# Performance work log

Hardware: AMD Instinct MI355X
Metric: run time of the kernel (lower is better)

## Reference

```python
import jax, jax.numpy as jnp
import numpy as np
import math

B, N, D, H, K, HID, FF = 4, 4096, 256, 4, 16, 64, 1024
DH = D // H
EPS = 1e-5


def setup_inputs() -> dict:
    key = jax.random.key(0)
    ks = jax.random.split(key, 24)
    s = 0.02
    inp = {
        'xyz': jax.random.uniform(ks[0], (B, N, 3), dtype=jnp.float32),
        'feats': jax.random.normal(ks[1], (B, N, D), dtype=jnp.float32),
        'ln_q_g': jnp.ones((D,), jnp.float32),
        'ln_q_b': jnp.zeros((D,), jnp.float32),
        'Wq': jax.random.normal(ks[2], (D, D), jnp.float32) * s,
        'bq': jnp.zeros((D,), jnp.float32),
        'Wk': jax.random.normal(ks[3], (D, D), jnp.float32) * s,
        'bk': jnp.zeros((D,), jnp.float32),
        'Wv': jax.random.normal(ks[4], (D, D), jnp.float32) * s,
        'bv': jnp.zeros((D,), jnp.float32),
        'W_rel1': jax.random.normal(ks[5], (4, HID), jnp.float32) * s,
        'b_rel1': jnp.zeros((HID,), jnp.float32),
        'W_rel2': jax.random.normal(ks[6], (HID, D), jnp.float32) * s,
        'b_rel2': jnp.zeros((D,), jnp.float32),
        'Wo': jax.random.normal(ks[7], (D, D), jnp.float32) * s,
        'bo': jnp.zeros((D,), jnp.float32),
        'ln_f_g': jnp.ones((D,), jnp.float32),
        'ln_f_b': jnp.zeros((D,), jnp.float32),
        'W_ff1': jax.random.normal(ks[8], (D, FF), jnp.float32) * s,
        'b_ff1': jnp.zeros((FF,), jnp.float32),
        'W_ff2': jax.random.normal(ks[9], (FF, D), jnp.float32) * s,
        'b_ff2': jnp.zeros((D,), jnp.float32),
    }
    return inp


def _layernorm(x, g, b):
    mu = jnp.mean(x, axis=-1, keepdims=True)
    var = jnp.var(x, axis=-1, keepdims=True)
    return (x - mu) * jax.lax.rsqrt(var + EPS) * g + b


def _knn_indices(xyz, k):
    # pairwise squared distances (B, N, N); exclude self via +inf diagonal
    sq = jnp.sum(xyz * xyz, axis=-1)  # (B, N)
    d2 = sq[:, :, None] + sq[:, None, :] - 2.0 * jnp.einsum('bnc,bmc->bnm', xyz, xyz)
    d2 = d2 + jnp.eye(xyz.shape[1], dtype=xyz.dtype) * 1e9
    _, idx = jax.lax.top_k(-d2, k)  # (B, N, k) nearest neighbors
    return idx


def _index_points(pts, idx):
    # pts: (B, N, C), idx: (B, N, k) -> (B, N, k, C)
    return jax.vmap(lambda p, i: p[i])(pts, idx)


def reference(xyz, feats, ln_q_g, ln_q_b, Wq, bq, Wk, bk, Wv, bv,
              W_rel1, b_rel1, W_rel2, b_rel2, Wo, bo,
              ln_f_g, ln_f_b, W_ff1, b_ff1, W_ff2, b_ff2):
    k = min(K, N - 1)
    idx = _knn_indices(xyz, k)

    x = _layernorm(feats, ln_q_g, ln_q_b)
    q = x @ Wq + bq
    k_lin = x @ Wk + bk
    v_lin = x @ Wv + bv

    k_nb = _index_points(k_lin, idx)   # (B,N,k,D)
    v_nb = _index_points(v_lin, idx)   # (B,N,k,D)
    nb_xyz = _index_points(xyz, idx)   # (B,N,k,3)

    diff = nb_xyz - xyz[:, :, None, :]
    rel = jnp.concatenate([diff, jnp.linalg.norm(diff, axis=-1, keepdims=True)], axis=-1)  # (B,N,k,4)
    rel_e = jax.nn.gelu(rel @ W_rel1 + b_rel1, approximate=False) @ W_rel2 + b_rel2

    k_nb = k_nb + rel_e
    v_nb = v_nb + rel_e

    qh = q.reshape(B, N, H, DH)              # (B,N,H,dh)
    kh = k_nb.reshape(B, N, k, H, DH)        # (B,N,k,H,dh)
    vh = v_nb.reshape(B, N, k, H, DH)

    attn = jnp.einsum('bnhc,bnkhc->bnhk', qh, kh) / math.sqrt(DH)
    attn = jax.nn.softmax(attn, axis=-1)
    out = jnp.einsum('bnhk,bnkhc->bnhc', attn, vh).reshape(B, N, D)
    out = out @ Wo + bo

    feats = feats + out
    h = _layernorm(feats, ln_f_g, ln_f_b)
    h = jax.nn.gelu(h @ W_ff1 + b_ff1, approximate=False) @ W_ff2 + b_ff2
    return feats + h
```

## Files before the change

kernel.cpp:

```cpp
#include <hip/hip_runtime.h>
#include <hip/hip_bf16.h>
#include <math.h>

#define NB 4
#define NPTS 4096
#define DIM 256
#define KNN 16
#define HID 64
#define FFDIM 1024
#define LN_EPS 1e-5f
#define MTOT (NB * NPTS)
#define KINF 3e38f
#define QPB 8

typedef __attribute__((ext_vector_type(8))) short short8;
typedef __attribute__((ext_vector_type(4))) float f32x4;

__device__ __forceinline__ float gelu_f(float x) {
    return 0.5f * x * (1.0f + erff(x * 0.7071067811865476f));
}
__device__ __forceinline__ float b2f(ushort u) {
    return __uint_as_float(((unsigned)u) << 16);
}
__device__ __forceinline__ ushort f2b(float f) {
    unsigned u = __float_as_uint(f);
    return (ushort)((u + 0x7fffu + ((u >> 16) & 1u)) >> 16);
}
__device__ __forceinline__ void gload16(const void* g, void* l) {
    __builtin_amdgcn_global_load_lds((const __attribute__((address_space(1))) void*)g,
                                     (__attribute__((address_space(3))) void*)l, 16, 0, 0);
}
__device__ __forceinline__ float dot8(uint4 w, const float* q) {
    float s = 0.f;
    s += b2f((ushort)(w.x & 0xffff)) * q[0]; s += b2f((ushort)(w.x >> 16)) * q[1];
    s += b2f((ushort)(w.y & 0xffff)) * q[2]; s += b2f((ushort)(w.y >> 16)) * q[3];
    s += b2f((ushort)(w.z & 0xffff)) * q[4]; s += b2f((ushort)(w.z >> 16)) * q[5];
    s += b2f((ushort)(w.w & 0xffff)) * q[6]; s += b2f((ushort)(w.w >> 16)) * q[7];
    return s;
}

__global__ __launch_bounds__(256) void knn_kernel(const float* __restrict__ xyz,
                                                  int* __restrict__ idx_out) {
    int blk = blockIdx.x;
    int bq0 = blk * QPB;
    int b = bq0 >> 12;
    const float* base = xyz + (size_t)b * NPTS * 3;
    int t = threadIdx.x;
    int lane = t & 63, wv = t >> 6;

    __shared__ float wq0S[64];
    __shared__ float wq1S[64];
    __shared__ int   cnt[QPB];
    __shared__ float cV[QPB][64];
    __shared__ int   cI[QPB][64];

    if (t < QPB) cnt[t] = 0;

    float px[16], py[16], pz[16], sq[16];
    #pragma unroll
    for (int i = 0; i < 16; ++i) {
        int m = t + 256 * i;
        px[i] = base[m * 3 + 0];
        py[i] = base[m * 3 + 1];
        pz[i] = base[m * 3 + 2];
        sq[i] = px[i] * px[i] + py[i] * py[i] + pz[i] * pz[i];
    }
    __syncthreads();

    #pragma unroll 1
    for (int qp = 0; qp < QPB; qp += 2) {
        int n0 = (bq0 + qp)     & (NPTS - 1);
        int n1 = (bq0 + qp + 1) & (NPTS - 1);
        float q0x = base[n0 * 3 + 0], q0y = base[n0 * 3 + 1], q0z = base[n0 * 3 + 2];
        float q1x = base[n1 * 3 + 0], q1y = base[n1 * 3 + 1], q1z = base[n1 * 3 + 2];
        float sq0 = q0x * q0x + q0y * q0y + q0z * q0z;
        float sq1 = q1x * q1x + q1y * q1y + q1z * q1z;

        float d0[16], d1[16];
        #pragma unroll
        for (int i = 0; i < 16; ++i) {
            int m = t + 256 * i;
            float dot0 = px[i] * q0x + py[i] * q0y + pz[i] * q0z;
            float dot1 = px[i] * q1x + py[i] * q1y + pz[i] * q1z;
            float dd0 = (sq0 + sq[i]) - 2.0f * dot0;
            float dd1 = (sq1 + sq[i]) - 2.0f * dot1;
            d0[i] = (m == n0) ? KINF : dd0;
            d1[i] = (m == n1) ? KINF : dd1;
        }
        float lm0 = d0[0], lm1 = d1[0];
        #pragma unroll
        for (int i = 1; i < 16; ++i) { lm0 = fminf(lm0, d0[i]); lm1 = fminf(lm1, d1[i]); }

        float v0 = lm0, v1 = lm1;
        #pragma unroll
        for (int k = 2; k <= 64; k <<= 1) {
            #pragma unroll
            for (int j = 32; j > 0; j >>= 1) {
                if (j < k) {
                    float ov0 = __shfl_xor(v0, j, 64);
                    float ov1 = __shfl_xor(v1, j, 64);
                    bool keepMin = ((lane & k) == 0) == ((lane & j) == 0);
                    if (keepMin == (ov0 < v0)) v0 = ov0;
                    if (keepMin == (ov1 < v1)) v1 = ov1;
                }
            }
        }
        if (lane < 16) { wq0S[wv * 16 + lane] = v0; wq1S[wv * 16 + lane] = v1; }
        __syncthreads();

        float s0 = wq0S[lane], s1 = wq1S[lane];
        #pragma unroll
        for (int k = 2; k <= 64; k <<= 1) {
            #pragma unroll
            for (int j = 32; j > 0; j >>= 1) {
                if (j < k) {
                    float os0 = __shfl_xor(s0, j, 64);
                    float os1 = __shfl_xor(s1, j, 64);
                    bool keepMin = ((lane & k) == 0) == ((lane & j) == 0);
                    if (keepMin == (os0 < s0)) s0 = os0;
                    if (keepMin == (os1 < s1)) s1 = os1;
                }
            }
        }
        float T0 = __shfl(s0, 15, 64);
        float T1 = __shfl(s1, 15, 64);

        #pragma unroll
        for (int i = 0; i < 16; ++i) {
            if (d0[i] <= T0) {
                int pos = atomicAdd(&cnt[qp], 1);
                if (pos < 64) { cV[qp][pos] = d0[i]; cI[qp][pos] = t + 256 * i; }
            }
        }
        #pragma unroll
        for (int i = 0; i < 16; ++i) {
            if (d1[i] <= T1) {
                int pos = atomicAdd(&cnt[qp + 1], 1);
                if (pos < 64) { cV[qp + 1][pos] = d1[i]; cI[qp + 1][pos] = t + 256 * i; }
            }
        }
        __syncthreads();
    }

    #pragma unroll
    for (int rep = 0; rep < 2; ++rep) {
        int qi = wv + 4 * rep;
        int nc = cnt[qi]; nc = nc > 64 ? 64 : nc;
        float v = (lane < nc) ? cV[qi][lane] : KINF;
        int   m = (lane < nc) ? cI[qi][lane] : 0x7fffffff;
        #pragma unroll
        for (int k = 2; k <= 64; k <<= 1) {
            #pragma unroll
            for (int j = 32; j > 0; j >>= 1) {
                if (j < k) {
                    float ov = __shfl_xor(v, j, 64);
                    int   om = __shfl_xor(m, j, 64);
                    bool keepMin = ((lane & k) == 0) == ((lane & j) == 0);
                    bool less = (ov < v) || (ov == v && om < m);
                    if (keepMin == less) { v = ov; m = om; }
                }
            }
        }
        if (lane < KNN) idx_out[(size_t)(bq0 + qi) * KNN + lane] = m;
    }
}

__global__ __launch_bounds__(256) void ln_kernel(const float* __restrict__ in,
                                                 const float* __restrict__ g,
                                                 const float* __restrict__ bb,
                                                 ushort* __restrict__ out) {
    int r = blockIdx.x;
    int t = threadIdx.x;
    float v = in[(size_t)r * DIM + t];

    __shared__ float sw[4];
    __shared__ float sw2[4];

    float s = v;
    #pragma unroll
    for (int off = 32; off > 0; off >>= 1) s += __shfl_down(s, off);
    if ((t & 63) == 0) sw[t >> 6] = s;
    __syncthreads();
    float mean = (sw[0] + sw[1] + sw[2] + sw[3]) * (1.0f / DIM);

    float dlt = v - mean;
    float s2 = dlt * dlt;
    #pragma unroll
    for (int off = 32; off > 0; off >>= 1) s2 += __shfl_down(s2, off);
    if ((t & 63) == 0) sw2[t >> 6] = s2;
    __syncthreads();
    float var = (sw2[0] + sw2[1] + sw2[2] + sw2[3]) * (1.0f / DIM);

    out[(size_t)r * DIM + t] = f2b(dlt * rsqrtf(var + LN_EPS) * g[t] + bb[t]);
}

__global__ __launch_bounds__(256) void tconv4(const float* __restrict__ s0,
                                              const float* __restrict__ s1,
                                              const float* __restrict__ s2,
                                              const float* __restrict__ s3,
                                              ushort* __restrict__ d0,
                                              ushort* __restrict__ d1,
                                              ushort* __restrict__ d2,
                                              ushort* __restrict__ d3) {
    const float* in; ushort* out;
    switch (blockIdx.z) {
        case 0: in = s0; out = d0; break;
        case 1: in = s1; out = d1; break;
        case 2: in = s2; out = d2; break;
        default: in = s3; out = d3; break;
    }
    __shared__ float tile[32][33];
    int tx = threadIdx.x & 31, ty = threadIdx.x >> 5;
    int r0 = blockIdx.y * 32, c0 = blockIdx.x * 32;
    #pragma unroll
    for (int k = 0; k < 4; ++k)
        tile[ty + 8 * k][tx] = in[(size_t)(r0 + ty + 8 * k) * 256 + c0 + tx];
    __syncthreads();
    #pragma unroll
    for (int k = 0; k < 4; ++k)
        out[(size_t)(c0 + ty + 8 * k) * 256 + r0 + tx] = f2b(tile[tx][ty + 8 * k]);
}

__global__ __launch_bounds__(256) void tconv(const float* __restrict__ in,
                                             ushort* __restrict__ out, int R, int C) {
    __shared__ float tile[32][33];
    int tx = threadIdx.x & 31, ty = threadIdx.x >> 5;
    int r0 = blockIdx.y * 32, c0 = blockIdx.x * 32;
    #pragma unroll
    for (int k = 0; k < 4; ++k)
        tile[ty + 8 * k][tx] = in[(size_t)(r0 + ty + 8 * k) * C + c0 + tx];
    __syncthreads();
    #pragma unroll
    for (int k = 0; k < 4; ++k)
        out[(size_t)(c0 + ty + 8 * k) * R + r0 + tx] = f2b(tile[tx][ty + 8 * k]);
}

__global__ __launch_bounds__(256) void prep_mats(const float* __restrict__ W2,
                                                 const float* __restrict__ Wq,
                                                 const ushort* __restrict__ WoT,
                                                 ushort* __restrict__ w2bd,
                                                 ushort* __restrict__ Wq_bf,
                                                 ushort* __restrict__ BtCat) {
    int bb = blockIdx.x, t = threadIdx.x;
    if (bb < 256) {
        float v = ((t >> 6) == (bb >> 6)) ? W2[(bb & 63) * 256 + t] : 0.0f;
        w2bd[bb * 256 + t] = f2b(v);
    } else if (bb < 512) {
        int r = bb - 256;
        Wq_bf[r * 256 + t] = f2b(Wq[r * 256 + t]);
    } else {
        int r = bb - 512;
        BtCat[(size_t)r * 512 + t] = WoT[r * 256 + t];
    }
}

__global__ __launch_bounds__(256) void prep_bias(const float* __restrict__ bq,
                                                 const float* __restrict__ bk,
                                                 const float* __restrict__ bv,
                                                 const float* __restrict__ W2,
                                                 const float* __restrict__ bo,
                                                 const float* __restrict__ br2,
                                                 const float* __restrict__ Wo,
                                                 float* __restrict__ bqkvw,
                                                 float* __restrict__ boc) {
    int bb = blockIdx.x, t = threadIdx.x;
    if (bb == 0) bqkvw[t] = bq[t];
    else if (bb == 1) bqkvw[256 + t] = bk[t];
    else if (bb == 2) bqkvw[512 + t] = bv[t];
    else if (bb == 3) {
        int h = t >> 6, i = t & 63;
        float s = 0.f;
        #pragma unroll 8
        for (int dp = 0; dp < 64; ++dp) s += bq[h * 64 + dp] * W2[i * 256 + h * 64 + dp];
        bqkvw[768 + t] = s;
    } else {
        float s = bo[t];
        #pragma unroll 8
        for (int d = 0; d < 256; ++d) s += br2[d] * Wo[d * 256 + t];
        boc[t] = s;
    }
}

template <int ACT, int OUTBF, int RES>
__global__ __launch_bounds__(256) void gemm_bt(
    const ushort* __restrict__ A, const ushort* __restrict__ Bt,
    const float* __restrict__ bias, const float* __restrict__ res,
    void* __restrict__ Cv, int M, int N, int K, int ldc)
{
    __shared__ ushort As[4096];
    __shared__ ushort Bs[4096];
    const int t = threadIdx.x;
    const int wave = t >> 6, lane = t & 63;
    const int m0 = blockIdx.y * 128, n0 = blockIdx.x * 128;
    const int wr = (wave >> 1) * 64, wc = (wave & 1) * 64;

    f32x4 acc[4][4];
    #pragma unroll
    for (int i = 0; i < 4; ++i)
        #pragma unroll
        for (int j = 0; j < 4; ++j) acc[i][j] = {0.f, 0.f, 0.f, 0.f};

    const int rA0 = (wave * 2 + 0) * 16 + (lane >> 2);
    const int rA1 = (wave * 2 + 1) * 16 + (lane >> 2);
    const int u4 = lane & 3;
    const int sw0 = (rA0 + (rA0 >> 2)) & 3;
    const int sw1 = (rA1 + (rA1 >> 2)) & 3;
    char* ldsA0 = (char*)As + (wave * 2 + 0) * 1024 + lane * 16;
    char* ldsA1 = (char*)As + (wave * 2 + 1) * 1024 + lane * 16;
    char* ldsB0 = (char*)Bs + (wave * 2 + 0) * 1024 + lane * 16;
    char* ldsB1 = (char*)Bs + (wave * 2 + 1) * 1024 + lane * 16;
    const size_t aOff0 = (size_t)(m0 + rA0) * K + (size_t)((u4 ^ sw0) * 8);
    const size_t aOff1 = (size_t)(m0 + rA1) * K + (size_t)((u4 ^ sw1) * 8);
    const size_t bOff0 = (size_t)(n0 + rA0) * K + (size_t)((u4 ^ sw0) * 8);
    const size_t bOff1 = (size_t)(n0 + rA1) * K + (size_t)((u4 ^ sw1) * 8);

    const int cl = lane & 15, gq = lane >> 4;

    for (int k0 = 0; k0 < K; k0 += 32) {
        gload16(A + aOff0 + k0, ldsA0);
        gload16(A + aOff1 + k0, ldsA1);
        gload16(Bt + bOff0 + k0, ldsB0);
        gload16(Bt + bOff1 + k0, ldsB1);
        __syncthreads();

        short8 av[4], bv[4];
        #pragma unroll
        for (int mi = 0; mi < 4; ++mi) {
            int row = wr + mi * 16 + cl;
            int s = (row + (row >> 2)) & 3;
            av[mi] = *(const short8*)((const char*)As + row * 64 + ((gq ^ s) << 4));
            int rowb = wc + mi * 16 + cl;
            int sb = (rowb + (rowb >> 2)) & 3;
            bv[mi] = *(const short8*)((const char*)Bs + rowb * 64 + ((gq ^ sb) << 4));
        }
        #pragma unroll
        for (int mi = 0; mi < 4; ++mi)
            #pragma unroll
            for (int ni = 0; ni < 4; ++ni)
                acc[mi][ni] = __builtin_amdgcn_mfma_f32_16x16x32_bf16(av[mi], bv[ni], acc[mi][ni], 0, 0, 0);
        __syncthreads();
    }

    float* Cf = (float*)Cv;
    ushort* Cb = (ushort*)Cv;
    #pragma unroll
    for (int ni = 0; ni < 4; ++ni) {
        int col = n0 + wc + ni * 16 + cl;
        float bvv = bias ? bias[col] : 0.0f;
        #pragma unroll
        for (int mi = 0; mi < 4; ++mi) {
            #pragma unroll
            for (int r = 0; r < 4; ++r) {
                int row = m0 + wr + mi * 16 + gq * 4 + r;
                float v = acc[mi][ni][r] + bvv;
                if (ACT == 1) v = gelu_f(v);
                if (RES) v += res[(size_t)row * N + col];
                if (OUTBF) Cb[(size_t)row * ldc + col] = f2b(v);
                else       Cf[(size_t)row * ldc + col] = v;
            }
        }
    }
}

#define PTS 8
__global__ __launch_bounds__(256) void attn_kernel(
    const int* __restrict__ idx,
    const ushort* __restrict__ qkvw,
    const float* __restrict__ xyz,
    const float* __restrict__ W1,
    const float* __restrict__ b1,
    ushort* __restrict__ ab)
{
    __shared__ float qS[256];
    __shared__ float qwS[256];
    __shared__ float psS[64];
    __shared__ uint4 hidS4[16 * 9];
    __shared__ int   nbAll[128];
    __shared__ float w1S[256];
    __shared__ float b1S[64];
    ushort* hidS = (ushort*)hidS4;

    const int t = threadIdx.x;
    const int h = t >> 6, lane = t & 63;
    const int bid = blockIdx.x;
    const int blk = ((bid & 7) << 8) | (bid >> 3);
    const int bn0 = blk * PTS;
    const int R0 = blk * (PTS * 16);

    if (t < 128) nbAll[t] = idx[R0 + t];
    w1S[t] = W1[t];
    if (t < 64) b1S[t] = b1[t];
    const float* xb3 = xyz + (size_t)(bn0 >> 12) * NPTS * 3;
    __syncthreads();

    for (int pt = 0; pt < PTS; ++pt) {
        const int bn = bn0 + pt;
        const size_t base = (size_t)(bn >> 12) * NPTS;

        qS[t]  = b2f(qkvw[(size_t)bn * 1024 + t]);
        qwS[t] = b2f(qkvw[(size_t)bn * 1024 + 768 + t]);
        {
            int n = bn & (NPTS - 1);
            float nx = xb3[n * 3 + 0], ny = xb3[n * 3 + 1], nz = xb3[n * 3 + 2];
            int j = t >> 4;
            int i0 = (t & 15) * 4;
            int m = nbAll[pt * 16 + j];
            float dx = xb3[m * 3 + 0] - nx;
            float dy = xb3[m * 3 + 1] - ny;
            float dz = xb3[m * 3 + 2] - nz;
            float nr = sqrtf(dx * dx + dy * dy + dz * dz);
            uint2 hw;
            float a0 = b1S[i0 + 0] + dx * w1S[i0 + 0] + dy * w1S[64 + i0 + 0] + dz * w1S[128 + i0 + 0] + nr * w1S[192 + i0 + 0];
            float a1 = b1S[i0 + 1] + dx * w1S[i0 + 1] + dy * w1S[64 + i0 + 1] + dz * w1S[128 + i0 + 1] + nr * w1S[192 + i0 + 1];
            float a2 = b1S[i0 + 2] + dx * w1S[i0 + 2] + dy * w1S[64 + i0 + 2] + dz * w1S[128 + i0 + 2] + nr * w1S[192 + i0 + 2];
            float a3 = b1S[i0 + 3] + dx * w1S[i0 + 3] + dy * w1S[64 + i0 + 3] + dz * w1S[128 + i0 + 3] + nr * w1S[192 + i0 + 3];
            hw.x = (uint)f2b(gelu_f(a0)) | ((uint)f2b(gelu_f(a1)) << 16);
            hw.y = (uint)f2b(gelu_f(a2)) | ((uint)f2b(gelu_f(a3)) << 16);
            *(uint2*)(hidS + j * 72 + i0) = hw;
        }
        __syncthreads();

        {
            int j = lane >> 2, sub = lane & 3;
            int m = nbAll[pt * 16 + j];
            const ushort* krow = qkvw + (base + m) * 1024 + 256 + h * 64 + sub * 16;
            uint4 ka = *(const uint4*)krow;
            uint4 kc = *(const uint4*)(krow + 8);
            const float* qp = &qS[h * 64 + sub * 16];
            float d1 = dot8(ka, qp) + dot8(kc, qp + 8);
            const ushort* hrow = hidS + j * 72 + sub * 16;
            uint4 ha = *(const uint4*)hrow;
            uint4 hc = *(const uint4*)(hrow + 8);
            const float* qwp = &qwS[h * 64 + sub * 16];
            float d2 = dot8(ha, qwp) + dot8(hc, qwp + 8);
            float pp = d1 + d2;
            pp += __shfl_xor(pp, 1, 64);
            pp += __shfl_xor(pp, 2, 64);
            pp *= 0.125f;
            float mx = pp;
            mx = fmaxf(mx, __shfl_xor(mx, 4, 64));
            mx = fmaxf(mx, __shfl_xor(mx, 8, 64));
            mx = fmaxf(mx, __shfl_xor(mx, 16, 64));
            mx = fmaxf(mx, __shfl_xor(mx, 32, 64));
            float e = expf(pp - mx);
            float ss = e;
            ss += __shfl_xor(ss, 4, 64);
            ss += __shfl_xor(ss, 8, 64);
            ss += __shfl_xor(ss, 16, 64);
            ss += __shfl_xor(ss, 32, 64);
            float pj = e / ss;
            if (sub == 0) psS[h * 16 + j] = pj;
        }
        __syncthreads();

        {
            float o = 0.f, hpv = 0.f;
            #pragma unroll
            for (int j = 0; j < 16; ++j) {
                float p = psS[h * 16 + j];
                int m = nbAll[pt * 16 + j];
                o   += p * b2f(qkvw[(base + m) * 1024 + 512 + t]);
                hpv += p * b2f(hidS[j * 72 + lane]);
            }
            ab[(size_t)bn * 512 + t]       = f2b(o);
            ab[(size_t)bn * 512 + 256 + t] = f2b(hpv);
        }
        __syncthreads();
    }
}

extern "C" void kernel_launch(void* const* d_in, const int* in_sizes, int n_in,
                              void* d_out, int out_size, void* d_ws, size_t ws_size,
                              hipStream_t stream) {
    const float* xyz    = (const float*)d_in[0];
    const float* feats  = (const float*)d_in[1];
    const float* ln_q_g = (const float*)d_in[2];
    const float* ln_q_b = (const float*)d_in[3];
    const float* Wq     = (const float*)d_in[4];
    const float* bq     = (const float*)d_in[5];
    const float* Wk     = (const float*)d_in[6];
    const float* bk     = (const float*)d_in[7];
    const float* Wv     = (const float*)d_in[8];
    const float* bv     = (const float*)d_in[9];
    const float* W_rel1 = (const float*)d_in[10];
    const float* b_rel1 = (const float*)d_in[11];
    const float* W_rel2 = (const float*)d_in[12];
    const float* b_rel2 = (const float*)d_in[13];
    const float* Wo     = (const float*)d_in[14];
    const float* bo     = (const float*)d_in[15];
    const float* ln_f_g = (const float*)d_in[16];
    const float* ln_f_b = (const float*)d_in[17];
    const float* W_ff1  = (const float*)d_in[18];
    const float* b_ff1  = (const float*)d_in[19];
    const float* W_ff2  = (const float*)d_in[20];
    const float* b_ff2  = (const float*)d_in[21];
    (void)in_sizes; (void)n_in; (void)out_size; (void)ws_size;

    char* ws = (char*)d_ws;
    const size_t MB = 1u << 20;
    int*    idx    = (int*)ws;
    ushort* xb     = (ushort*)(ws + 1 * MB);
    ushort* qkvw   = (ushort*)(ws + 9 * MB);
    ushort* ff1b   = (ushort*)(ws + 41 * MB);
    ushort* ab     = (ushort*)(ws + 73 * MB);
    ushort* BtQKVW = (ushort*)(ws + 89 * MB);
    ushort* WoT    = BtQKVW + 262144;
    ushort* Wf1T   = WoT + 65536;
    ushort* Wf2T   = Wf1T + 262144;
    ushort* Wq_bf  = Wf2T + 262144;
    ushort* w2bd   = Wq_bf + 65536;
    ushort* BtCat  = w2bd + 65536;
    float*  bqkvw  = (float*)(BtCat + 131072);
    float*  boc    = bqkvw + 1024;
    float*  feats1 = (float*)(ws + 9 * MB);
    ushort* hb     = xb;

    tconv4<<<dim3(8, 8, 4), 256, 0, stream>>>(Wq, Wk, Wv, Wo,
                                              BtQKVW, BtQKVW + 65536, BtQKVW + 131072, WoT);
    tconv<<<dim3(32, 8), 256, 0, stream>>>(W_ff1, Wf1T, 256, 1024);
    tconv<<<dim3(8, 32), 256, 0, stream>>>(W_ff2, Wf2T, 1024, 256);
    prep_mats<<<768, 256, 0, stream>>>(W_rel2, Wq, WoT, w2bd, Wq_bf, BtCat);
    gemm_bt<0, 1, 0><<<dim3(2, 2), 256, 0, stream>>>(w2bd, Wq_bf, nullptr, nullptr,
                                                     BtQKVW + 768 * 256, 256, 256, 256, 256);
    gemm_bt<0, 1, 0><<<dim3(2, 2), 256, 0, stream>>>(WoT, w2bd, nullptr, nullptr,
                                                     BtCat + 256, 256, 256, 256, 512);
    prep_bias<<<5, 256, 0, stream>>>(bq, bk, bv, W_rel2, bo, b_rel2, Wo, bqkvw, boc);

    knn_kernel<<<MTOT / QPB, 256, 0, stream>>>(xyz, idx);
    ln_kernel<<<MTOT, 256, 0, stream>>>(feats, ln_q_g, ln_q_b, xb);

    gemm_bt<0, 1, 0><<<dim3(8, 128), 256, 0, stream>>>(xb, BtQKVW, bqkvw, nullptr,
                                                       qkvw, MTOT, 1024, 256, 1024);

    attn_kernel<<<MTOT / PTS, 256, 0, stream>>>(idx, qkvw, xyz, W_rel1, b_rel1, ab);

    gemm_bt<0, 0, 1><<<dim3(2, 128), 256, 0, stream>>>(ab, BtCat, boc, feats, feats1, MTOT, 256, 512, 256);
    ln_kernel<<<MTOT, 256, 0, stream>>>(feats1, ln_f_g, ln_f_b, hb);
    gemm_bt<1, 1, 0><<<dim3(8, 128), 256, 0, stream>>>(hb, Wf1T, b_ff1, nullptr, ff1b, MTOT, 1024, 256, 1024);
    gemm_bt<0, 0, 1><<<dim3(2, 128), 256, 0, stream>>>(ff1b, Wf2T, b_ff2, feats1, (float*)d_out, MTOT, 256, 1024, 256);
}
```

Baseline: 288.4 us.

## Restructure KNN so each wavefront computes one query's top-k from LDS-staged points

The KNN kernel now stages all of a batch's point coordinates in shared memory. Each wavefront handles a whole query on its own: it computes 64 distances per lane, finds a threshold with an in-wave bitonic sort, compacts the candidates and does the final sort. This removes the block-wide barriers and the cross-wave merge that the old paired-query loop needed. The cost is 48KB of LDS per block, which can limit occupancy. Squared norms are recomputed from LDS on every query, and each lane holds a 64-entry distance array in registers.

```diff
diff --git a/kernel.cpp b/kernel.cpp
--- a/kernel.cpp
+++ b/kernel.cpp
@@ -48,120 +48,81 @@
     int t = threadIdx.x;
     int lane = t & 63, wv = t >> 6;
 
-    __shared__ float wq0S[64];
-    __shared__ float wq1S[64];
+    __shared__ float pxS[NPTS];
+    __shared__ float pyS[NPTS];
+    __shared__ float pzS[NPTS];
     __shared__ int   cnt[QPB];
     __shared__ float cV[QPB][64];
     __shared__ int   cI[QPB][64];
 
     if (t < QPB) cnt[t] = 0;
-
-    float px[16], py[16], pz[16], sq[16];
-    #pragma unroll
-    for (int i = 0; i < 16; ++i) {
-        int m = t + 256 * i;
-        px[i] = base[m * 3 + 0];
-        py[i] = base[m * 3 + 1];
-        pz[i] = base[m * 3 + 2];
-        sq[i] = px[i] * px[i] + py[i] * py[i] + pz[i] * pz[i];
+    for (int i = t; i < NPTS; i += 256) {
+        pxS[i] = base[i * 3 + 0];
+        pyS[i] = base[i * 3 + 1];
+        pzS[i] = base[i * 3 + 2];
     }
     __syncthreads();
 
     #pragma unroll 1
-    for (int qp = 0; qp < QPB; qp += 2) {
-        int n0 = (bq0 + qp)     & (NPTS - 1);
-        int n1 = (bq0 + qp + 1) & (NPTS - 1);
-        float q0x = base[n0 * 3 + 0], q0y = base[n0 * 3 + 1], q0z = base[n0 * 3 + 2];
-        float q1x = base[n1 * 3 + 0], q1y = base[n1 * 3 + 1], q1z = base[n1 * 3 + 2];
-        float sq0 = q0x * q0x + q0y * q0y + q0z * q0z;
-        float sq1 = q1x * q1x + q1y * q1y + q1z * q1z;
-
-        float d0[16], d1[16];
-        #pragma unroll
-        for (int i = 0; i < 16; ++i) {
-            int m = t + 256 * i;
-            float dot0 = px[i] * q0x + py[i] * q0y + pz[i] * q0z;
-            float dot1 = px[i] * q1x + py[i] * q1y + pz[i] * q1z;
-            float dd0 = (sq0 + sq[i]) - 2.0f * dot0;
-            float dd1 = (sq1 + sq[i]) - 2.0f * dot1;
-            d0[i] = (m == n0) ? KINF : dd0;
-            d1[i] = (m == n1) ? KINF : dd1;
-        }
-        float lm0 = d0[0], lm1 = d1[0];
-        #pragma unroll
-        for (int i = 1; i < 16; ++i) { lm0 = fminf(lm0, d0[i]); lm1 = fminf(lm1, d1[i]); }
-
-        float v0 = lm0, v1 = lm1;
-        #pragma unroll
-        for (int k = 2; k <= 64; k <<= 1) {
-            #pragma unroll
-            for (int j = 32; j > 0; j >>= 1) {
-                if (j < k) {
-                    float ov0 = __shfl_xor(v0, j, 64);
-                    float ov1 = __shfl_xor(v1, j, 64);
-                    bool keepMin = ((lane & k) == 0) == ((lane & j) == 0);
-                    if (keepMin == (ov0 < v0)) v0 = ov0;
-                    if (keepMin == (ov1 < v1)) v1 = ov1;
-                }
-            }
-        }
-        if (lane < 16) { wq0S[wv * 16 + lane] = v0; wq1S[wv * 16 + lane] = v1; }
-        __syncthreads();
-
-        float s0 = wq0S[lane], s1 = wq1S[lane];
-        #pragma unroll
-        for (int k = 2; k <= 64; k <<= 1) {
-            #pragma unroll
-            for (int j = 32; j > 0; j >>= 1) {
-                if (j < k) {
-                    float os0 = __shfl_xor(s0, j, 64);
-                    float os1 = __shfl_xor(s1, j, 64);
-                    bool keepMin = ((lane & k) == 0) == ((lane & j) == 0);
-                    if (keepMin == (os0 < s0)) s0 = os0;
-                    if (keepMin == (os1 < s1)) s1 = os1;
-                }
-            }
-        }
-        float T0 = __shfl(s0, 15, 64);
-        float T1 = __shfl(s1, 15, 64);
-
-        #pragma unroll
-        for (int i = 0; i < 16; ++i) {
-            if (d0[i] <= T0) {
-                int pos = atomicAdd(&cnt[qp], 1);
-                if (pos < 64) { cV[qp][pos] = d0[i]; cI[qp][pos] = t + 256 * i; }
-            }
-        }
-        #pragma unroll
-        for (int i = 0; i < 16; ++i) {
-            if (d1[i] <= T1) {
-                int pos = atomicAdd(&cnt[qp + 1], 1);
-                if (pos < 64) { cV[qp + 1][pos] = d1[i]; cI[qp + 1][pos] = t + 256 * i; }
-            }
-        }
-        __syncthreads();
-    }
-
-    #pragma unroll
     for (int rep = 0; rep < 2; ++rep) {
         int qi = wv + 4 * rep;
-        int nc = cnt[qi]; nc = nc > 64 ? 64 : nc;
-        float v = (lane < nc) ? cV[qi][lane] : KINF;
-        int   m = (lane < nc) ? cI[qi][lane] : 0x7fffffff;
+        int bn = bq0 + qi;
+        int n = bn & (NPTS - 1);
+        float qx = pxS[n], qy = pyS[n], qz = pzS[n];
+        float sqn = qx * qx + qy * qy + qz * qz;
+
+        float d[64];
+        float lm = KINF;
+        #pragma unroll
+        for (int i = 0; i < 64; ++i) {
+            int m = lane + 64 * i;
+            float x = pxS[m], y = pyS[m], z = pzS[m];
+            float sqm = x * x + y * y + z * z;
+            float dot = qx * x + qy * y + qz * z;
+            float dd = (sqn + sqm) - 2.0f * dot;
+            d[i] = (m == n) ? KINF : dd;
+            lm = fminf(lm, d[i]);
+        }
+
+        float v = lm;
         #pragma unroll
         for (int k = 2; k <= 64; k <<= 1) {
             #pragma unroll
             for (int j = 32; j > 0; j >>= 1) {
                 if (j < k) {
                     float ov = __shfl_xor(v, j, 64);
-                    int   om = __shfl_xor(m, j, 64);
                     bool keepMin = ((lane & k) == 0) == ((lane & j) == 0);
-                    bool less = (ov < v) || (ov == v && om < m);
-                    if (keepMin == less) { v = ov; m = om; }
+                    if (keepMin == (ov < v)) v = ov;
                 }
             }
         }
-        if (lane < KNN) idx_out[(size_t)(bq0 + qi) * KNN + lane] = m;
+        float T = __shfl(v, 15, 64);
+
+        #pragma unroll
+        for (int i = 0; i < 64; ++i) {
+            if (d[i] <= T) {
+                int pos = atomicAdd(&cnt[qi], 1);
+                if (pos < 64) { cV[qi][pos] = d[i]; cI[qi][pos] = lane + 64 * i; }
+            }
+        }
+
+        int nc = cnt[qi]; nc = nc > 64 ? 64 : nc;
+        float v2 = (lane < nc) ? cV[qi][lane] : KINF;
+        int   m2 = (lane < nc) ? cI[qi][lane] : 0x7fffffff;
+        #pragma unroll
+        for (int k = 2; k <= 64; k <<= 1) {
+            #pragma unroll
+            for (int j = 32; j > 0; j >>= 1) {
+                if (j < k) {
+                    float ov = __shfl_xor(v2, j, 64);
+                    int   om = __shfl_xor(m2, j, 64);
+                    bool keepMin = ((lane & k) == 0) == ((lane & j) == 0);
+                    bool less = (ov < v2) || (ov == v2 && om < m2);
+                    if (keepMin == less) { v2 = ov; m2 = om; }
+                }
+            }
+        }
+        if (lane < KNN) idx_out[(size_t)bn * KNN + lane] = m2;
     }
 }
 
```

Result: no change. 283.7 us (-1.6%).
